# Optimization experiments

Measured on AMD Instinct MI355X. Metric: run time of the kernel, lower is better.

The kernel has to match this reference:

```python
import jax, jax.numpy as jnp
import numpy as np

N_NODES = 100_000
N_EDGES = 1_600_000
HID = 64
LAYERS = 3
MAX_ATOM = 100
BATCH = 16


def setup_inputs() -> dict:
    key = jax.random.key(0)
    ks = jax.random.split(key, 24)
    s = 0.05  # weight scale
    inp = {
        "x": jax.random.normal(ks[0], (N_NODES, 3), dtype=jnp.float32),
        "z": jax.random.randint(ks[1], (N_NODES,), 0, MAX_ATOM),
        "t": jax.random.uniform(ks[2], (BATCH, 1), dtype=jnp.float32),
        "edge_index": jax.random.randint(ks[3], (2, N_EDGES), 0, N_NODES),
        # atom embedding table
        "emb": jax.random.normal(ks[4], (MAX_ATOM, HID)) * s,
        # time embedding MLP: Linear(1,H), SiLU, Linear(H,H)
        "t_w1": jax.random.normal(ks[5], (1, HID)) * s,
        "t_b1": jnp.zeros((HID,)),
        "t_w2": jax.random.normal(ks[6], (HID, HID)) * s,
        "t_b2": jnp.zeros((HID,)),
        # per-layer EGNN params, stacked over layers
        # edge MLP: Linear(2H+1, H), SiLU, Linear(H, H), SiLU
        "e_w1": jax.random.normal(ks[7], (LAYERS, 2 * HID + 1, HID)) * s,
        "e_b1": jnp.zeros((LAYERS, HID)),
        "e_w2": jax.random.normal(ks[8], (LAYERS, HID, HID)) * s,
        "e_b2": jnp.zeros((LAYERS, HID)),
        # coord MLP: Linear(H, H), SiLU, Linear(H, 1)
        "c_w1": jax.random.normal(ks[9], (LAYERS, HID, HID)) * s,
        "c_b1": jnp.zeros((LAYERS, HID)),
        "c_w2": jax.random.normal(ks[10], (LAYERS, HID, 1)) * s,
        "c_b2": jnp.zeros((LAYERS, 1)),
        # node MLP: Linear(2H, H), SiLU, Linear(H, H), residual
        "n_w1": jax.random.normal(ks[11], (LAYERS, 2 * HID, HID)) * s,
        "n_b1": jnp.zeros((LAYERS, HID)),
        "n_w2": jax.random.normal(ks[12], (LAYERS, HID, HID)) * s,
        "n_b2": jnp.zeros((LAYERS, HID)),
    }
    return inp


def reference(x, z, t, edge_index, emb,
              t_w1, t_b1, t_w2, t_b2,
              e_w1, e_b1, e_w2, e_b2,
              c_w1, c_b1, c_w2, c_b2,
              n_w1, n_b1, n_w2, n_b2):
    silu = jax.nn.silu
    n = x.shape[0]
    # atom embedding + global time conditioning
    h = emb[z]                                           # (N, H)
    t_emb = silu(t @ t_w1 + t_b1) @ t_w2 + t_b2          # (B, H)
    h = h + jnp.mean(t_emb, axis=0, keepdims=True)
    src, dst = edge_index[0], edge_index[1]
    for l in range(LAYERS):
        diff = x[dst] - x[src]                           # (E, 3)
        d2 = jnp.sum(diff * diff, axis=-1, keepdims=True)  # (E, 1)
        ef = jnp.concatenate([h[dst], h[src], d2], axis=-1)  # (E, 2H+1)
        m = silu(silu(ef @ e_w1[l] + e_b1[l]) @ e_w2[l] + e_b2[l])  # (E, H)
        cw = silu(m @ c_w1[l] + c_b1[l]) @ c_w2[l] + c_b2[l]        # (E, 1)
        x = x + jax.ops.segment_sum(diff * cw, dst, num_segments=n)
        agg = jax.ops.segment_sum(m, dst, num_segments=n)           # (N, H)
        nf = jnp.concatenate([h, agg], axis=-1)                     # (N, 2H)
        h = h + (silu(nf @ n_w1[l] + n_b1[l]) @ n_w2[l] + n_b2[l])
    return x
```

## Files before the change

kernel.cpp:

```cpp
#include <hip/hip_runtime.h>

typedef __attribute__((ext_vector_type(8))) short s8v;
typedef __attribute__((ext_vector_type(4))) float f32x4;

#define MFMA16(A,B,C) __builtin_amdgcn_mfma_f32_16x16x32_bf16((A),(B),(C),0,0,0)

__device__ __forceinline__ float b2f(unsigned short s){
  union { unsigned u; float f; } v; v.u = ((unsigned)s) << 16; return v.f;
}
__device__ __forceinline__ unsigned short f2b(float f){
  union { float f; unsigned u; } v; v.f = f;
  return (unsigned short)((v.u + 0x8000u) >> 16);
}
__device__ __forceinline__ float siluf(float x){
  return x * __builtin_amdgcn_rcpf(1.f + __expf(-x));
}


__global__ void hist_kernel(const int* __restrict__ dst, int* __restrict__ deg, int E){
  int i = blockIdx.x*256 + threadIdx.x;
  if (i < E) atomicAdd(&deg[dst[i]], 1);
}

__global__ void scan1_kernel(const int* __restrict__ deg, int* __restrict__ rp,
                             int* __restrict__ bsum, int N){
  __shared__ int s[256];
  const int base = blockIdx.x*1024;
  const int t = threadIdx.x;
  int v[4];
  #pragma unroll
  for (int j = 0; j < 4; ++j){
    int idx = base + t*4 + j;
    int dv = (idx < N) ? deg[idx] : 0;
    v[j] = (dv + 3) & ~3;
  }
  const int tsum = v[0]+v[1]+v[2]+v[3];
  s[t] = tsum;
  __syncthreads();
  for (int off = 1; off < 256; off <<= 1){
    int x = (t >= off) ? s[t-off] : 0;
    __syncthreads();
    s[t] += x;
    __syncthreads();
  }
  const int incl = s[t];
  if (t == 255) bsum[blockIdx.x] = incl;
  int run = incl - tsum;
  #pragma unroll
  for (int j = 0; j < 4; ++j){
    int idx = base + t*4 + j;
    if (idx < N) rp[idx] = run;
    run += v[j];
  }
}

__global__ void scan2_kernel(int* __restrict__ bsum, int nb){
  __shared__ int s[256];
  const int t = threadIdx.x;
  const int v = (t < nb) ? bsum[t] : 0;
  s[t] = v;
  __syncthreads();
  for (int off = 1; off < 256; off <<= 1){
    int x = (t >= off) ? s[t-off] : 0;
    __syncthreads();
    s[t] += x;
    __syncthreads();
  }
  if (t < nb) bsum[t] = s[t] - v;
}

__global__ void scan3_kernel(int* __restrict__ rp, const int* __restrict__ bsum,
                             const int* __restrict__ deg, int N){
  int i = blockIdx.x*256 + threadIdx.x;
  if (i < N){
    int v = rp[i] + bsum[i >> 10];
    rp[i] = v;
    if (i == N-1) rp[N] = v + ((deg[i] + 3) & ~3);
  }
}

__global__ void scatter_kernel(const int* __restrict__ src, const int* __restrict__ dst,
                               const int* __restrict__ rp, int* __restrict__ cursor,
                               int* __restrict__ csr_src, int E){
  int i = blockIdx.x*256 + threadIdx.x;
  if (i < E){
    const int d = dst[i];
    const int pos = rp[d] + atomicAdd(&cursor[d], 1);
    csr_src[pos] = src[i];
  }
}

__global__ void slot_build_kernel(const int* __restrict__ rp, const int* __restrict__ deg,
                                  int* __restrict__ slot_meta, int* __restrict__ csr_src,
                                  int N){
  int n = blockIdx.x*256 + threadIdx.x;
  if (n < N){
    const int base = rp[n];
    const int d = deg[n];
    const int ns = (d + 3) >> 2;
    const int s0 = base >> 2;
    for (int k = 0; k < ns; ++k){
      int c = d - k*4; c = (c > 4) ? 4 : c;
      slot_meta[s0 + k] = n | (c << 28);
    }
    for (int i = d; i < ns*4; ++i) csr_src[base + i] = n;
  }
  if (n == 0){
    const int S  = rp[N] >> 2;
    const int S4 = (S + 3) & ~3;
    for (int s = S; s < S4; ++s){
      slot_meta[s] = 0;
      for (int r = 0; r < 4; ++r) csr_src[s*4 + r] = 0;
    }
  }
}


__global__ void tmean_kernel(const float* __restrict__ t,
                             const float* __restrict__ tw1,
                             const float* __restrict__ tb1,
                             const float* __restrict__ tw2,
                             const float* __restrict__ tb2,
                             float* __restrict__ tmean){
  __shared__ __align__(16) float s1[16*64];
  int j = threadIdx.x;
  float w1 = tw1[j], bb1 = tb1[j];
  for (int b = 0; b < 16; ++b)
    s1[b*64 + j] = siluf(t[b] * w1 + bb1);
  __syncthreads();
  float acc = 0.f;
  for (int b = 0; b < 16; ++b)
    for (int k = 0; k < 64; ++k)
      acc += s1[b*64 + k] * tw2[k*64 + j];
  tmean[j] = tb2[j] + acc * (1.f/16.f);
}

__global__ void init_h_kernel(const int* __restrict__ z,
                              const float* __restrict__ emb,
                              const float* __restrict__ tmean,
                              float* __restrict__ hf,
                              unsigned short* __restrict__ hb, int N){
  int i = blockIdx.x*256 + threadIdx.x;
  if (i >= N*64) return;
  int j = i & 63;
  int n = i >> 6;
  float v = emb[z[n]*64 + j] + tmean[j];
  hf[i] = v;
  hb[i] = f2b(v);
}


__global__ __launch_bounds__(512) void p12_kernel(
    const unsigned short* __restrict__ hb,
    const float* __restrict__ ew1, const float* __restrict__ eb1,
    unsigned short* __restrict__ P1, unsigned short* __restrict__ P2,
    int layer, int N)
{
  __shared__ __align__(16) short w1a[64*72];
  __shared__ __align__(16) short w1b[64*72];
  __shared__ __align__(16) float b1s[64];

  const int tid = threadIdx.x;
  const float* w1g = ew1 + layer*129*64;
  for (int idx = tid; idx < 64*64; idx += 512){
    int k = idx >> 6, n = idx & 63;
    w1a[n*72 + k] = (short)f2b(w1g[k*64 + n]);
    w1b[n*72 + k] = (short)f2b(w1g[(64 + k)*64 + n]);
  }
  if (tid < 64) b1s[tid] = eb1[layer*64 + tid];
  __syncthreads();

  const int lane = tid & 63;
  const int wv = tid >> 6;
  const int q = lane >> 4;
  const int n16 = lane & 15;

  const int ntile = N >> 4;
  const int step = gridDim.x * 8;
  for (int t = blockIdx.x*8 + wv; t < ntile; t += step){
    const int row = t*16 + n16;
    const s8v* ph = (const s8v*)(hb + row*64);
    const s8v a0 = ph[q];
    const s8v a1 = ph[4+q];
    #pragma unroll
    for (int nt = 0; nt < 4; ++nt){
      const s8v* wa = (const s8v*)&w1a[(nt*16 + n16)*72];
      const s8v* wb = (const s8v*)&w1b[(nt*16 + n16)*72];
      f32x4 aA = {0.f,0.f,0.f,0.f};
      aA = MFMA16(a0, wa[q],   aA);
      aA = MFMA16(a1, wa[4+q], aA);
      f32x4 aB = {0.f,0.f,0.f,0.f};
      aB = MFMA16(a0, wb[q],   aB);
      aB = MFMA16(a1, wb[4+q], aB);
      const float bb = b1s[nt*16 + n16];
      #pragma unroll
      for (int r = 0; r < 4; ++r){
        const int o = (t*16 + q*4 + r)*64 + nt*16 + n16;
        P1[o] = f2b(aA[r] + bb);
        P2[o] = f2b(aB[r]);
      }
    }
  }
}


__global__ __launch_bounds__(512) void edge_tile_kernel(
    const int* __restrict__ rp, const int* __restrict__ csr_src,
    const int* __restrict__ slot_meta,
    const float* __restrict__ x_in, float* __restrict__ x_out,
    const unsigned short* __restrict__ P1, const unsigned short* __restrict__ P2,
    float* __restrict__ aggf,
    const float* __restrict__ ew1,
    const float* __restrict__ ew2, const float* __restrict__ eb2,
    const float* __restrict__ cw1, const float* __restrict__ cb1,
    const float* __restrict__ cw2, const float* __restrict__ cb2,
    int layer, int do_agg, int N)
{
  __shared__ __align__(16) short wT2[64*72];
  __shared__ __align__(16) short wc1T[64*72];
  __shared__ __align__(16) short sc[8][16*72];
  __shared__ __align__(16) float sdiff[8][48];

  const int tid = threadIdx.x;
  const float* w2g = ew2 + layer*64*64;
  const float* c1g = cw1 + layer*64*64;
  for (int idx = tid; idx < 64*64; idx += 512){
    int k = idx >> 6, n = idx & 63;
    wT2[n*72 + k]  = (short)f2b(w2g[k*64 + n]);
    wc1T[n*72 + k] = (short)f2b(c1g[k*64 + n]);
  }

  const int lane = tid & 63;
  const int wv = tid >> 6;
  const int q = lane >> 4;
  const int n16 = lane & 15;
  short* mysc = sc[wv];
  float* mydiff = sdiff[wv];

  const float* wlg = ew1 + layer*129*64 + 128*64;
  float wl_lo[8], wl_hi[8];
  #pragma unroll
  for (int j = 0; j < 8; ++j){
    wl_lo[j] = wlg[q*8 + j];
    wl_hi[j] = wlg[32 + q*8 + j];
  }
  float be2r[4], bc1r[4], cw2r[4];
  #pragma unroll
  for (int nt = 0; nt < 4; ++nt){
    be2r[nt] = eb2[layer*64 + nt*16 + n16];
    bc1r[nt] = cb1[layer*64 + nt*16 + n16];
    cw2r[nt] = cw2[layer*64 + nt*16 + n16];
  }
  const float cb2s = cb2[layer];
  __syncthreads();

  const int T = (rp[N] + 15) >> 4;
  const int nwave = gridDim.x * 8;
  for (int t = blockIdx.x*8 + wv; t < T; t += nwave){
    const int mi = slot_meta[t*4 + (n16 >> 2)];
    const int di = mi & 0x0FFFFFFF;
    const int si = csr_src[t*16 + n16];
    const float dx = x_in[di*3+0] - x_in[si*3+0];
    const float dy = x_in[di*3+1] - x_in[si*3+1];
    const float dz = x_in[di*3+2] - x_in[si*3+2];
    const float d2 = dx*dx + dy*dy + dz*dz;
    if (q == 0){ mydiff[n16*3+0]=dx; mydiff[n16*3+1]=dy; mydiff[n16*3+2]=dz; }

    const s8v* pd = (const s8v*)(P1 + (size_t)di*64);
    const s8v lo1 = pd[q];
    const s8v hi1 = pd[4+q];
    const s8v* ps = (const s8v*)(P2 + (size_t)si*64);
    const s8v lo2 = ps[q];
    const s8v hi2 = ps[4+q];

    s8v alo, ahi;
    #pragma unroll
    for (int j = 0; j < 8; ++j){
      const float v0 = b2f((unsigned short)lo1[j]) + b2f((unsigned short)lo2[j]) + d2*wl_lo[j];
      alo[j] = (short)f2b(siluf(v0));
      const float v1 = b2f((unsigned short)hi1[j]) + b2f((unsigned short)hi2[j]) + d2*wl_hi[j];
      ahi[j] = (short)f2b(siluf(v1));
    }

    f32x4 acc2[4];
    #pragma unroll
    for (int nt = 0; nt < 4; ++nt){
      const s8v* wb = (const s8v*)&wT2[(nt*16 + n16)*72];
      f32x4 a = {0.f,0.f,0.f,0.f};
      a = MFMA16(alo, wb[q],   a);
      a = MFMA16(ahi, wb[4+q], a);
      acc2[nt] = a;
    }

    const int mo = slot_meta[t*4 + q];
    const int dn = mo & 0x0FFFFFFF;
    const int cnt = (int)(((unsigned)mo) >> 28);

    float colsum[4] = {0.f,0.f,0.f,0.f};
    #pragma unroll
    for (int nt = 0; nt < 4; ++nt){
      const float bb = be2r[nt];
      #pragma unroll
      for (int r = 0; r < 4; ++r){
        const float mv = siluf(acc2[nt][r] + bb);
        mysc[(q*4 + r)*72 + nt*16 + n16] = (short)f2b(mv);
        colsum[nt] += (r < cnt) ? mv : 0.f;
      }
    }
    __builtin_amdgcn_wave_barrier();
    const s8v* srd = (const s8v*)&mysc[n16*72];
    const s8v m0 = srd[q];
    const s8v m1 = srd[4+q];
    __builtin_amdgcn_wave_barrier();

    float pr[4] = {0.f,0.f,0.f,0.f};
    #pragma unroll
    for (int nt = 0; nt < 4; ++nt){
      const s8v* wb = (const s8v*)&wc1T[(nt*16 + n16)*72];
      f32x4 a = {0.f,0.f,0.f,0.f};
      a = MFMA16(m0, wb[q],   a);
      a = MFMA16(m1, wb[4+q], a);
      const float bc = bc1r[nt];
      const float wc2 = cw2r[nt];
      #pragma unroll
      for (int r = 0; r < 4; ++r) pr[r] += siluf(a[r] + bc) * wc2;
    }
    #pragma unroll
    for (int off = 1; off < 16; off <<= 1){
      #pragma unroll
      for (int r = 0; r < 4; ++r) pr[r] += __shfl_xor(pr[r], off, 64);
    }
    float xacc0 = 0.f, xacc1 = 0.f, xacc2 = 0.f;
    #pragma unroll
    for (int r = 0; r < 4; ++r){
      const float cwv = pr[r] + cb2s;
      xacc0 += mydiff[(q*4 + r)*3 + 0] * cwv;
      xacc1 += mydiff[(q*4 + r)*3 + 1] * cwv;
      xacc2 += mydiff[(q*4 + r)*3 + 2] * cwv;
    }

    const int dnb = __shfl_xor(dn, 16, 64);
    const bool same = (dnb == dn);
    #pragma unroll
    for (int nt = 0; nt < 4; ++nt){
      const float o = __shfl_xor(colsum[nt], 16, 64);
      if (same) colsum[nt] += o;
    }
    const float o0 = __shfl_xor(xacc0, 16, 64);
    const float o1 = __shfl_xor(xacc1, 16, 64);
    const float o2 = __shfl_xor(xacc2, 16, 64);
    if (same){ xacc0 += o0; xacc1 += o1; xacc2 += o2; }

    const bool writer = ((q & 1) == 0) || !same;
    if (do_agg && writer){
      #pragma unroll
      for (int nt = 0; nt < 4; ++nt)
        atomicAdd(&aggf[(size_t)dn*64 + nt*16 + n16], colsum[nt]);
    }
    if (writer && n16 < 3){
      const float v = (n16 == 0) ? xacc0 : (n16 == 1) ? xacc1 : xacc2;
      atomicAdd(&x_out[dn*3 + n16], v);
    }
  }
}


__global__ __launch_bounds__(512) void node_p12_kernel(
    unsigned short* __restrict__ hb, float* __restrict__ hf,
    const float* __restrict__ aggf,
    const float* __restrict__ nw1, const float* __restrict__ nb1,
    const float* __restrict__ nw2, const float* __restrict__ nb2,
    const float* __restrict__ ew1, const float* __restrict__ eb1,
    unsigned short* __restrict__ P1, unsigned short* __restrict__ P2,
    int layer, int N)
{
  __shared__ __align__(16) short wT1[64*136];
  __shared__ __align__(16) short wT2[64*72];
  __shared__ __align__(16) short w1a[64*72];
  __shared__ __align__(16) short w1b[64*72];
  __shared__ __align__(16) short sc[8][16*72];
  __shared__ __align__(16) float b1s[64];
  __shared__ __align__(16) float b2s[64];
  __shared__ __align__(16) float eb1s[64];

  const int tid = threadIdx.x;
  const float* w1g = nw1 + layer*128*64;
  const float* w2g = nw2 + layer*64*64;
  const float* e1g = ew1 + (layer+1)*129*64;
  for (int idx = tid; idx < 64*128; idx += 512){
    int k = idx >> 6, n = idx & 63;
    wT1[n*136 + k] = (short)f2b(w1g[k*64 + n]);
  }
  for (int idx = tid; idx < 64*64; idx += 512){
    int k = idx >> 6, n = idx & 63;
    wT2[n*72 + k] = (short)f2b(w2g[k*64 + n]);
    w1a[n*72 + k] = (short)f2b(e1g[k*64 + n]);
    w1b[n*72 + k] = (short)f2b(e1g[(64 + k)*64 + n]);
  }
  if (tid < 64){
    b1s[tid]  = nb1[layer*64 + tid];
    b2s[tid]  = nb2[layer*64 + tid];
    eb1s[tid] = eb1[(layer+1)*64 + tid];
  }
  __syncthreads();

  const int lane = tid & 63;
  const int wv = tid >> 6;
  const int q = lane >> 4;
  const int n16 = lane & 15;
  short* mysc = sc[wv];

  const int ntile = N >> 4;
  const int step = gridDim.x * 8;
  for (int t = blockIdx.x*8 + wv; t < ntile; t += step){
    const int row = t*16 + n16;
    const s8v* ph = (const s8v*)(hb + row*64);
    const s8v a0 = ph[q];
    const s8v a1 = ph[4+q];
    const f32x4* pa = (const f32x4*)(aggf + (size_t)row*64);
    const f32x4 u0 = pa[2*q];
    const f32x4 u1 = pa[2*q+1];
    const f32x4 u2 = pa[8+2*q];
    const f32x4 u3 = pa[9+2*q];
    s8v a2, a3;
    #pragma unroll
    for (int j = 0; j < 4; ++j){
      a2[j]   = (short)f2b(u0[j]);
      a2[4+j] = (short)f2b(u1[j]);
      a3[j]   = (short)f2b(u2[j]);
      a3[4+j] = (short)f2b(u3[j]);
    }

    #pragma unroll
    for (int nt = 0; nt < 4; ++nt){
      const s8v* wb = (const s8v*)&wT1[(nt*16 + n16)*136];
      f32x4 a = {0.f,0.f,0.f,0.f};
      a = MFMA16(a0, wb[q],    a);
      a = MFMA16(a1, wb[4+q],  a);
      a = MFMA16(a2, wb[8+q],  a);
      a = MFMA16(a3, wb[12+q], a);
      const float bb = b1s[nt*16 + n16];
      #pragma unroll
      for (int r = 0; r < 4; ++r)
        mysc[(q*4 + r)*72 + nt*16 + n16] = (short)f2b(siluf(a[r] + bb));
    }
    __builtin_amdgcn_wave_barrier();
    const s8v* srd = (const s8v*)&mysc[n16*72];
    const s8v g0 = srd[q];
    const s8v g1 = srd[4+q];
    __builtin_amdgcn_wave_barrier();

    #pragma unroll
    for (int nt = 0; nt < 4; ++nt){
      const s8v* wb = (const s8v*)&wT2[(nt*16 + n16)*72];
      f32x4 a = {0.f,0.f,0.f,0.f};
      a = MFMA16(g0, wb[q],   a);
      a = MFMA16(g1, wb[4+q], a);
      const float bb = b2s[nt*16 + n16];
      #pragma unroll
      for (int r = 0; r < 4; ++r){
        const int idx = (t*16 + q*4 + r)*64 + nt*16 + n16;
        const float hv = hf[idx] + a[r] + bb;
        hf[idx] = hv;
        const unsigned short hvb = f2b(hv);
        hb[idx] = hvb;
        mysc[(q*4 + r)*72 + nt*16 + n16] = (short)hvb;
      }
    }
    __builtin_amdgcn_wave_barrier();
    const s8v h0 = srd[q];
    const s8v h1 = srd[4+q];
    __builtin_amdgcn_wave_barrier();

    #pragma unroll
    for (int nt = 0; nt < 4; ++nt){
      const s8v* wa = (const s8v*)&w1a[(nt*16 + n16)*72];
      const s8v* wb = (const s8v*)&w1b[(nt*16 + n16)*72];
      f32x4 aA = {0.f,0.f,0.f,0.f};
      aA = MFMA16(h0, wa[q],   aA);
      aA = MFMA16(h1, wa[4+q], aA);
      f32x4 aB = {0.f,0.f,0.f,0.f};
      aB = MFMA16(h0, wb[q],   aB);
      aB = MFMA16(h1, wb[4+q], aB);
      const float bb = eb1s[nt*16 + n16];
      #pragma unroll
      for (int r = 0; r < 4; ++r){
        const int o = (t*16 + q*4 + r)*64 + nt*16 + n16;
        P1[o] = f2b(aA[r] + bb);
        P2[o] = f2b(aB[r]);
      }
    }
  }
}


extern "C" void kernel_launch(void* const* d_in, const int* in_sizes, int n_in,
                              void* d_out, int out_size, void* d_ws, size_t ws_size,
                              hipStream_t stream)
{
  const float* x0   = (const float*)d_in[0];
  const int*   z    = (const int*)d_in[1];
  const float* tc   = (const float*)d_in[2];
  const int*   ei   = (const int*)d_in[3];
  const float* embc = (const float*)d_in[4];
  const float* tw1c = (const float*)d_in[5];
  const float* tb1c = (const float*)d_in[6];
  const float* tw2c = (const float*)d_in[7];
  const float* tb2c = (const float*)d_in[8];
  const float* ew1c = (const float*)d_in[9];
  const float* eb1c = (const float*)d_in[10];
  const float* ew2c = (const float*)d_in[11];
  const float* eb2c = (const float*)d_in[12];
  const float* cw1c = (const float*)d_in[13];
  const float* cb1c = (const float*)d_in[14];
  const float* cw2c = (const float*)d_in[15];
  const float* cb2c = (const float*)d_in[16];
  const float* nw1c = (const float*)d_in[17];
  const float* nb1c = (const float*)d_in[18];
  const float* nw2c = (const float*)d_in[19];
  const float* nb2c = (const float*)d_in[20];

  const int N = in_sizes[1];
  const int E = in_sizes[3] / 2;
  const int* srcp = ei;
  const int* dstp = ei + E;

  char* p = (char*)d_ws;
  auto alloc = [&](size_t bytes) -> void* {
    void* r = (void*)p; p += (bytes + 255) & ~(size_t)255; return r;
  };
  float* hf            = (float*)alloc((size_t)N*64*4);
  unsigned short* hbuf = (unsigned short*)alloc((size_t)N*64*2);
  float* aggf          = (float*)alloc((size_t)N*64*4);
  unsigned short* P1   = (unsigned short*)alloc((size_t)N*64*2);
  unsigned short* P2   = (unsigned short*)alloc((size_t)N*64*2);
  float* xa            = (float*)alloc((size_t)N*3*4);
  float* xb            = (float*)alloc((size_t)N*3*4);
  float* tmean         = (float*)alloc(64*4);
  int*   degcur        = (int*)alloc((size_t)2*N*4);
  int*   deg           = degcur;
  int*   cursor        = degcur + N;
  int*   rowp          = (int*)alloc((size_t)(N+1)*4);
  int*   bsum          = (int*)alloc(256*4);
  int*   csr_src       = (int*)alloc(((size_t)E + 3*(size_t)N + 64)*4);
  int*   slot_meta     = (int*)alloc(((size_t)E/4 + (size_t)N + 16)*4);

  tmean_kernel<<<1, 64, 0, stream>>>(tc, tw1c, tb1c, tw2c, tb2c, tmean);
  init_h_kernel<<<(N*64 + 255)/256, 256, 0, stream>>>(z, embc, tmean, hf, hbuf, N);

  (void)hipMemsetAsync(degcur, 0, (size_t)2*N*4, stream);
  hist_kernel<<<(E + 255)/256, 256, 0, stream>>>(dstp, deg, E);
  const int nb = (N + 1023)/1024;
  scan1_kernel<<<nb, 256, 0, stream>>>(deg, rowp, bsum, N);
  scan2_kernel<<<1, 256, 0, stream>>>(bsum, nb);
  scan3_kernel<<<(N + 255)/256, 256, 0, stream>>>(rowp, bsum, deg, N);
  scatter_kernel<<<(E + 255)/256, 256, 0, stream>>>(srcp, dstp, rowp, cursor, csr_src, E);
  slot_build_kernel<<<(N + 255)/256, 256, 0, stream>>>(rowp, deg, slot_meta, csr_src, N);

  p12_kernel<<<512, 512, 0, stream>>>(hbuf, ew1c, eb1c, P1, P2, 0, N);

  const float* xc = x0;
  float* xnexts[3] = {xa, xb, (float*)d_out};
  for (int l = 0; l < 3; ++l){
    float* xout = xnexts[l];
    (void)hipMemcpyAsync(xout, xc, (size_t)N*3*4, hipMemcpyDeviceToDevice, stream);
    if (l < 2) (void)hipMemsetAsync(aggf, 0, (size_t)N*64*4, stream);
    edge_tile_kernel<<<1024, 512, 0, stream>>>(rowp, csr_src, slot_meta, xc, xout,
        P1, P2, aggf,
        ew1c, ew2c, eb2c, cw1c, cb1c, cw2c, cb2c, l, (l < 2) ? 1 : 0, N);
    if (l < 2)
      node_p12_kernel<<<512, 512, 0, stream>>>(hbuf, hf, aggf,
          nw1c, nb1c, nw2c, nb2c, ew1c, eb1c, P1, P2, l, N);
    xc = xout;
  }
}
```

Before: 826.2 us.

## Software-pipeline edge tile loop by prefetching next tile's gathers

The edge tile loop now issues the gathers for the next tile (slot metadata, source index, endpoint coordinates, and P1/P2 rows) while the current tile's MFMA and reduction work runs, hiding gather latency. It also stores the per-edge diff in a structure-of-arrays layout so it can be read back as vector loads, adds a min-waves occupancy hint to the launch bounds, and reduces the grid from 1024 to 768 blocks. The cost is higher register pressure from the prefetched values held across the loop body, which the occupancy hint may force into spills.

New measurement: 953.2 us. 15.4% more time.

```diff
diff --git a/kernel.cpp b/kernel.cpp
--- a/kernel.cpp
+++ b/kernel.cpp
@@ -204,7 +204,7 @@
 }
 
 
-__global__ __launch_bounds__(512) void edge_tile_kernel(
+__global__ __launch_bounds__(512, 6) void edge_tile_kernel(
     const int* __restrict__ rp, const int* __restrict__ csr_src,
     const int* __restrict__ slot_meta,
     const float* __restrict__ x_in, float* __restrict__ x_out,
@@ -256,22 +256,38 @@
 
   const int T = (rp[N] + 15) >> 4;
   const int nwave = gridDim.x * 8;
-  for (int t = blockIdx.x*8 + wv; t < T; t += nwave){
-    const int mi = slot_meta[t*4 + (n16 >> 2)];
-    const int di = mi & 0x0FFFFFFF;
-    const int si = csr_src[t*16 + n16];
-    const float dx = x_in[di*3+0] - x_in[si*3+0];
-    const float dy = x_in[di*3+1] - x_in[si*3+1];
-    const float dz = x_in[di*3+2] - x_in[si*3+2];
+  int t = blockIdx.x*8 + wv;
+  if (t >= T) return;
+
+  int mo;
+  float xd0, xd1, xd2, xs0, xs1, xs2;
+  s8v lo1, hi1, lo2, hi2;
+  {
+    const int mi0 = slot_meta[t*4 + (n16 >> 2)];
+    mo = slot_meta[t*4 + q];
+    const int si0 = csr_src[t*16 + n16];
+    const int di0 = mi0 & 0x0FFFFFFF;
+    xd0 = x_in[di0*3+0]; xd1 = x_in[di0*3+1]; xd2 = x_in[di0*3+2];
+    xs0 = x_in[si0*3+0]; xs1 = x_in[si0*3+1]; xs2 = x_in[si0*3+2];
+    const s8v* pd = (const s8v*)(P1 + (size_t)di0*64);
+    lo1 = pd[q]; hi1 = pd[4+q];
+    const s8v* ps = (const s8v*)(P2 + (size_t)si0*64);
+    lo2 = ps[q]; hi2 = ps[4+q];
+  }
+
+  while (true){
+    const int t2 = t + nwave;
+    const int tp = (t2 < T) ? t2 : t;
+
+    const int mi2 = slot_meta[tp*4 + (n16 >> 2)];
+    const int mo2 = slot_meta[tp*4 + q];
+    const int si2 = csr_src[tp*16 + n16];
+
+    const float dx = xd0 - xs0;
+    const float dy = xd1 - xs1;
+    const float dz = xd2 - xs2;
     const float d2 = dx*dx + dy*dy + dz*dz;
-    if (q == 0){ mydiff[n16*3+0]=dx; mydiff[n16*3+1]=dy; mydiff[n16*3+2]=dz; }
-
-    const s8v* pd = (const s8v*)(P1 + (size_t)di*64);
-    const s8v lo1 = pd[q];
-    const s8v hi1 = pd[4+q];
-    const s8v* ps = (const s8v*)(P2 + (size_t)si*64);
-    const s8v lo2 = ps[q];
-    const s8v hi2 = ps[4+q];
+    if (q == 0){ mydiff[n16] = dx; mydiff[16+n16] = dy; mydiff[32+n16] = dz; }
 
     s8v alo, ahi;
     #pragma unroll
@@ -292,7 +308,14 @@
       acc2[nt] = a;
     }
 
-    const int mo = slot_meta[t*4 + q];
+    const int di2 = mi2 & 0x0FFFFFFF;
+    const float nxd0 = x_in[di2*3+0], nxd1 = x_in[di2*3+1], nxd2 = x_in[di2*3+2];
+    const float nxs0 = x_in[si2*3+0], nxs1 = x_in[si2*3+1], nxs2 = x_in[si2*3+2];
+    const s8v* npd = (const s8v*)(P1 + (size_t)di2*64);
+    const s8v nlo1 = npd[q], nhi1 = npd[4+q];
+    const s8v* nps = (const s8v*)(P2 + (size_t)si2*64);
+    const s8v nlo2 = nps[q], nhi2 = nps[4+q];
+
     const int dn = mo & 0x0FFFFFFF;
     const int cnt = (int)(((unsigned)mo) >> 28);
 
@@ -330,13 +353,16 @@
       #pragma unroll
       for (int r = 0; r < 4; ++r) pr[r] += __shfl_xor(pr[r], off, 64);
     }
+    const f32x4 dfx = *(const f32x4*)&mydiff[q*4];
+    const f32x4 dfy = *(const f32x4*)&mydiff[16 + q*4];
+    const f32x4 dfz = *(const f32x4*)&mydiff[32 + q*4];
     float xacc0 = 0.f, xacc1 = 0.f, xacc2 = 0.f;
     #pragma unroll
     for (int r = 0; r < 4; ++r){
       const float cwv = pr[r] + cb2s;
-      xacc0 += mydiff[(q*4 + r)*3 + 0] * cwv;
-      xacc1 += mydiff[(q*4 + r)*3 + 1] * cwv;
-      xacc2 += mydiff[(q*4 + r)*3 + 2] * cwv;
+      xacc0 += dfx[r] * cwv;
+      xacc1 += dfy[r] * cwv;
+      xacc2 += dfz[r] * cwv;
     }
 
     const int dnb = __shfl_xor(dn, 16, 64);
@@ -361,6 +387,13 @@
       const float v = (n16 == 0) ? xacc0 : (n16 == 1) ? xacc1 : xacc2;
       atomicAdd(&x_out[dn*3 + n16], v);
     }
+
+    if (t2 >= T) break;
+    t = t2;
+    mo = mo2;
+    xd0 = nxd0; xd1 = nxd1; xd2 = nxd2;
+    xs0 = nxs0; xs1 = nxs1; xs2 = nxs2;
+    lo1 = nlo1; hi1 = nhi1; lo2 = nlo2; hi2 = nhi2;
   }
 }
 
@@ -565,7 +598,7 @@
     float* xout = xnexts[l];
     (void)hipMemcpyAsync(xout, xc, (size_t)N*3*4, hipMemcpyDeviceToDevice, stream);
     if (l < 2) (void)hipMemsetAsync(aggf, 0, (size_t)N*64*4, stream);
-    edge_tile_kernel<<<1024, 512, 0, stream>>>(rowp, csr_src, slot_meta, xc, xout,
+    edge_tile_kernel<<<768, 512, 0, stream>>>(rowp, csr_src, slot_meta, xc, xout,
         P1, P2, aggf,
         ew1c, ew2c, eb2c, cw1c, cb1c, cw2c, cb2c, l, (l < 2) ? 1 : 0, N);
     if (l < 2)
```

## Fold memsets, copies and small setup kernels into neighboring kernels

Applied to the files above, without the earlier changes.

Merges scatter and slot build into one kernel, and folds degree zeroing into the time-embedding kernel. The initial aggf zeroing moves into init_h, and the inter-layer aggf zeroing and x copy move into node_p12. This removes several separate memset/memcpy operations and kernel launches from the stream. The cost is extra stores inside the node kernel, and correctness now depends on tile coverage and on ordering across kernels.

New measurement: 817.9 us. No clear change (-1.0%).

```diff
diff --git a/kernel.cpp b/kernel.cpp
--- a/kernel.cpp
+++ b/kernel.cpp
@@ -79,33 +79,28 @@
   }
 }
 
-__global__ void scatter_kernel(const int* __restrict__ src, const int* __restrict__ dst,
-                               const int* __restrict__ rp, int* __restrict__ cursor,
-                               int* __restrict__ csr_src, int E){
+__global__ void scatter_slot_kernel(const int* __restrict__ src, const int* __restrict__ dst,
+                                    const int* __restrict__ rp, int* __restrict__ cursor,
+                                    int* __restrict__ csr_src, int* __restrict__ slot_meta,
+                                    const int* __restrict__ deg, int E, int N){
   int i = blockIdx.x*256 + threadIdx.x;
   if (i < E){
     const int d = dst[i];
     const int pos = rp[d] + atomicAdd(&cursor[d], 1);
     csr_src[pos] = src[i];
   }
-}
-
-__global__ void slot_build_kernel(const int* __restrict__ rp, const int* __restrict__ deg,
-                                  int* __restrict__ slot_meta, int* __restrict__ csr_src,
-                                  int N){
-  int n = blockIdx.x*256 + threadIdx.x;
-  if (n < N){
-    const int base = rp[n];
-    const int d = deg[n];
+  if (i < N){
+    const int base = rp[i];
+    const int d = deg[i];
     const int ns = (d + 3) >> 2;
     const int s0 = base >> 2;
     for (int k = 0; k < ns; ++k){
       int c = d - k*4; c = (c > 4) ? 4 : c;
-      slot_meta[s0 + k] = n | (c << 28);
-    }
-    for (int i = d; i < ns*4; ++i) csr_src[base + i] = n;
-  }
-  if (n == 0){
+      slot_meta[s0 + k] = i | (c << 28);
+    }
+    for (int j = d; j < ns*4; ++j) csr_src[base + j] = i;
+  }
+  if (i == 0){
     const int S  = rp[N] >> 2;
     const int S4 = (S + 3) & ~3;
     for (int s = S; s < S4; ++s){
@@ -116,30 +111,40 @@
 }
 
 
-__global__ void tmean_kernel(const float* __restrict__ t,
-                             const float* __restrict__ tw1,
-                             const float* __restrict__ tb1,
-                             const float* __restrict__ tw2,
-                             const float* __restrict__ tb2,
-                             float* __restrict__ tmean){
-  __shared__ __align__(16) float s1[16*64];
-  int j = threadIdx.x;
-  float w1 = tw1[j], bb1 = tb1[j];
-  for (int b = 0; b < 16; ++b)
-    s1[b*64 + j] = siluf(t[b] * w1 + bb1);
-  __syncthreads();
-  float acc = 0.f;
-  for (int b = 0; b < 16; ++b)
-    for (int k = 0; k < 64; ++k)
-      acc += s1[b*64 + k] * tw2[k*64 + j];
-  tmean[j] = tb2[j] + acc * (1.f/16.f);
+__global__ void tmean_zero_kernel(const float* __restrict__ t,
+                                  const float* __restrict__ tw1,
+                                  const float* __restrict__ tb1,
+                                  const float* __restrict__ tw2,
+                                  const float* __restrict__ tb2,
+                                  float* __restrict__ tmean,
+                                  int* __restrict__ degcur, int n2){
+  for (int k = blockIdx.x*256 + threadIdx.x; k < n2; k += gridDim.x*256)
+    degcur[k] = 0;
+  if (blockIdx.x == 0){
+    __shared__ __align__(16) float s1[16*64];
+    const int j = threadIdx.x & 63;
+    const int grp = threadIdx.x >> 6;
+    const float w1 = tw1[j], bb1 = tb1[j];
+    #pragma unroll
+    for (int b = grp*4; b < grp*4 + 4; ++b)
+      s1[b*64 + j] = siluf(t[b] * w1 + bb1);
+    __syncthreads();
+    if (threadIdx.x < 64){
+      float acc = 0.f;
+      for (int b = 0; b < 16; ++b)
+        for (int k = 0; k < 64; ++k)
+          acc += s1[b*64 + k] * tw2[k*64 + j];
+      tmean[j] = tb2[j] + acc * (1.f/16.f);
+    }
+  }
 }
 
 __global__ void init_h_kernel(const int* __restrict__ z,
                               const float* __restrict__ emb,
                               const float* __restrict__ tmean,
                               float* __restrict__ hf,
-                              unsigned short* __restrict__ hb, int N){
+                              unsigned short* __restrict__ hb,
+                              float* __restrict__ aggf, int N){
   int i = blockIdx.x*256 + threadIdx.x;
   if (i >= N*64) return;
   int j = i & 63;
@@ -147,6 +152,7 @@
   float v = emb[z[n]*64 + j] + tmean[j];
   hf[i] = v;
   hb[i] = f2b(v);
+  aggf[i] = 0.f;
 }
 
 
@@ -367,12 +373,13 @@
 
 __global__ __launch_bounds__(512) void node_p12_kernel(
     unsigned short* __restrict__ hb, float* __restrict__ hf,
-    const float* __restrict__ aggf,
+    float* __restrict__ aggf,
     const float* __restrict__ nw1, const float* __restrict__ nb1,
     const float* __restrict__ nw2, const float* __restrict__ nb2,
     const float* __restrict__ ew1, const float* __restrict__ eb1,
     unsigned short* __restrict__ P1, unsigned short* __restrict__ P2,
-    int layer, int N)
+    const float* __restrict__ xsrc, float* __restrict__ xdst,
+    int layer, int do_zero, int N)
 {
   __shared__ __align__(16) short wT1[64*136];
   __shared__ __align__(16) short wT2[64*72];
@@ -430,6 +437,12 @@
       a3[j]   = (short)f2b(u2[j]);
       a3[4+j] = (short)f2b(u3[j]);
     }
+    if (do_zero){
+      const f32x4 zz = {0.f,0.f,0.f,0.f};
+      f32x4* pw = (f32x4*)(aggf + (size_t)row*64);
+      pw[2*q] = zz; pw[2*q+1] = zz; pw[8+2*q] = zz; pw[9+2*q] = zz;
+    }
+    if (lane < 48) xdst[t*48 + lane] = xsrc[t*48 + lane];
 
     #pragma unroll
     for (int nt = 0; nt < 4; ++nt){
@@ -545,32 +558,32 @@
   int*   csr_src       = (int*)alloc(((size_t)E + 3*(size_t)N + 64)*4);
   int*   slot_meta     = (int*)alloc(((size_t)E/4 + (size_t)N + 16)*4);
 
-  tmean_kernel<<<1, 64, 0, stream>>>(tc, tw1c, tb1c, tw2c, tb2c, tmean);
-  init_h_kernel<<<(N*64 + 255)/256, 256, 0, stream>>>(z, embc, tmean, hf, hbuf, N);
-
-  (void)hipMemsetAsync(degcur, 0, (size_t)2*N*4, stream);
+  tmean_zero_kernel<<<512, 256, 0, stream>>>(tc, tw1c, tb1c, tw2c, tb2c,
+                                             tmean, degcur, 2*N);
+  init_h_kernel<<<(N*64 + 255)/256, 256, 0, stream>>>(z, embc, tmean, hf, hbuf, aggf, N);
+
   hist_kernel<<<(E + 255)/256, 256, 0, stream>>>(dstp, deg, E);
   const int nb = (N + 1023)/1024;
   scan1_kernel<<<nb, 256, 0, stream>>>(deg, rowp, bsum, N);
   scan2_kernel<<<1, 256, 0, stream>>>(bsum, nb);
   scan3_kernel<<<(N + 255)/256, 256, 0, stream>>>(rowp, bsum, deg, N);
-  scatter_kernel<<<(E + 255)/256, 256, 0, stream>>>(srcp, dstp, rowp, cursor, csr_src, E);
-  slot_build_kernel<<<(N + 255)/256, 256, 0, stream>>>(rowp, deg, slot_meta, csr_src, N);
+  scatter_slot_kernel<<<(E + 255)/256, 256, 0, stream>>>(srcp, dstp, rowp, cursor,
+                                                         csr_src, slot_meta, deg, E, N);
 
   p12_kernel<<<512, 512, 0, stream>>>(hbuf, ew1c, eb1c, P1, P2, 0, N);
 
   const float* xc = x0;
   float* xnexts[3] = {xa, xb, (float*)d_out};
+  (void)hipMemcpyAsync(xa, x0, (size_t)N*3*4, hipMemcpyDeviceToDevice, stream);
   for (int l = 0; l < 3; ++l){
     float* xout = xnexts[l];
-    (void)hipMemcpyAsync(xout, xc, (size_t)N*3*4, hipMemcpyDeviceToDevice, stream);
-    if (l < 2) (void)hipMemsetAsync(aggf, 0, (size_t)N*64*4, stream);
     edge_tile_kernel<<<1024, 512, 0, stream>>>(rowp, csr_src, slot_meta, xc, xout,
         P1, P2, aggf,
         ew1c, ew2c, eb2c, cw1c, cb1c, cw2c, cb2c, l, (l < 2) ? 1 : 0, N);
     if (l < 2)
       node_p12_kernel<<<512, 512, 0, stream>>>(hbuf, hf, aggf,
-          nw1c, nb1c, nw2c, nb2c, ew1c, eb1c, P1, P2, l, N);
+          nw1c, nb1c, nw2c, nb2c, ew1c, eb1c, P1, P2,
+          xout, xnexts[l+1], l, (l == 0) ? 1 : 0, N);
     xc = xout;
   }
 }
```
